# Kernel tuning notes

Measured on AMD Instinct MI355X. Metric: run time of the kernel, lower is better.

Reference implementation:

```python
import jax, jax.numpy as jnp
import numpy as np

N = 10000   # nodes
E = 50000   # edges
C = 64      # in_channels / hidden
OUT = 64    # final out_channels


def _conv(x, src, dst, edge_attr, nn_w, nn_b, lin_w, bias):
    # edge MLP -> per-edge weight matrix [E, C, C]
    W = (edge_attr @ nn_w + nn_b).reshape(-1, C, C)
    x_j = x[src]                                   # gather source features [E, C]
    msg = jnp.einsum('ei,eio->eo', x_j, W)         # batched matvec [E, C]
    out = jax.ops.segment_sum(msg, dst, num_segments=N)  # scatter-add to targets
    out = out + x @ lin_w + bias                   # root weight + bias
    return out


def setup_inputs() -> dict:
    key = jax.random.key(0)
    ks = jax.random.split(key, 13)
    s = 1.0 / np.sqrt(C).astype(np.float32)
    return {
        'feature': jax.random.normal(ks[0], (N, C), dtype=jnp.float32),
        'edge_index': jax.random.randint(ks[1], (2, E), 0, N),
        'edge_attr': jax.random.normal(ks[2], (E, C), dtype=jnp.float32),
        # conv layer 0 (in=64 -> out=64)
        'nn_w0': jax.random.normal(ks[3], (C, C * C), dtype=jnp.float32) * s,
        'nn_b0': jnp.zeros((C * C,), dtype=jnp.float32),
        'lin_w0': jax.random.normal(ks[4], (C, C), dtype=jnp.float32) * s,
        'bias0': jnp.zeros((C,), dtype=jnp.float32),
        # conv layer 1 (64 -> 64)
        'nn_w1': jax.random.normal(ks[5], (C, C * C), dtype=jnp.float32) * s,
        'nn_b1': jnp.zeros((C * C,), dtype=jnp.float32),
        'lin_w1': jax.random.normal(ks[6], (C, C), dtype=jnp.float32) * s,
        'bias1': jnp.zeros((C,), dtype=jnp.float32),
        # final linear 64 -> 64
        'fin_w': jax.random.normal(ks[7], (C, OUT), dtype=jnp.float32) * s,
        'fin_b': jnp.zeros((OUT,), dtype=jnp.float32),
    }


def reference(feature, edge_index, edge_attr,
              nn_w0, nn_b0, lin_w0, bias0,
              nn_w1, nn_b1, lin_w1, bias1,
              fin_w, fin_b):
    src, dst = edge_index[0], edge_index[1]  # PyG flow: source_to_target
    x = jax.nn.relu(_conv(feature, src, dst, edge_attr, nn_w0, nn_b0, lin_w0, bias0))
    x = jax.nn.relu(_conv(x, src, dst, edge_attr, nn_w1, nn_b1, lin_w1, bias1))
    return x @ fin_w + fin_b
```

## Files before the change

kernel.cpp:

```cpp
#include <hip/hip_runtime.h>


#define NNODES 10000
#define NEDGES 50000
#define CH 64
#define NSTAGES 65
#define MW 64

typedef _Float16 f16;
typedef f16 f16x8 __attribute__((ext_vector_type(8)));
typedef float f32x4 __attribute__((ext_vector_type(4)));


__global__ void zero_kernel(int* __restrict__ hist, int* __restrict__ cursor) {
    int idx = blockIdx.x * 256 + threadIdx.x;
    if (idx < NNODES) { hist[idx] = 0; cursor[idx] = 0; }
}

__global__ void hist_kernel(const int* __restrict__ ei, int* __restrict__ hist) {
    int e = blockIdx.x * 256 + threadIdx.x;
    if (e < NEDGES) atomicAdd(&hist[ei[NEDGES + e]], 1);
}

__global__ __launch_bounds__(1024)
void scan_kernel(const int* __restrict__ hist, int* __restrict__ start) {
    __shared__ int buf[1024];
    int t = threadIdx.x;
    int base = t * 10;
    int loc[10];
    int s = 0;
#pragma unroll
    for (int i = 0; i < 10; ++i) {
        int n = base + i;
        int v = (n < NNODES) ? hist[n] : 0;
        loc[i] = s; s += v;
    }
    buf[t] = s;
    __syncthreads();
    for (int off = 1; off < 1024; off <<= 1) {
        int add = (t >= off) ? buf[t - off] : 0;
        __syncthreads();
        buf[t] += add;
        __syncthreads();
    }
    int ebase = buf[t] - s;
#pragma unroll
    for (int i = 0; i < 10; ++i) {
        int n = base + i;
        if (n < NNODES) start[n] = ebase + loc[i];
    }
    if (t == 1023) start[NNODES] = buf[1023];
}

__global__ void perm_kernel(const int* __restrict__ ei,
                            const int* __restrict__ start,
                            int* __restrict__ cursor,
                            int* __restrict__ eperm,
                            int* __restrict__ esrc) {
    int e = blockIdx.x * 256 + threadIdx.x;
    if (e < NEDGES) {
        int d = ei[NEDGES + e];
        int pos = start[d] + atomicAdd(&cursor[d], 1);
        eperm[pos] = e;
        esrc[pos]  = ei[e];
    }
}

__global__ void eagather_kernel(const float* __restrict__ ea,
                                const int* __restrict__ eperm,
                                float* __restrict__ eas) {
    int idx = blockIdx.x * 256 + threadIdx.x;
    if (idx >= NEDGES * 16) return;
    int p = idx >> 4, quad = idx & 15;
    int e = eperm[p];
    *(float4*)(eas + (size_t)p * 64 + quad * 4) =
        *(const float4*)(ea + (size_t)e * 64 + quad * 4);
}

__global__ void pack_b_kernel(const float* __restrict__ nw0, const float* __restrict__ nb0,
                              const float* __restrict__ nw1, const float* __restrict__ nb1,
                              f16* __restrict__ Bp0, f16* __restrict__ Bp1) {
    int idx = blockIdx.x * 256 + threadIdx.x;
    if (idx >= 2 * NSTAGES * 2048) return;
    int layer = (idx >= NSTAGES * 2048) ? 1 : 0;
    int r = idx - layer * NSTAGES * 2048;
    const float* nn_w = layer ? nw1 : nw0;
    const float* nn_b = layer ? nb1 : nb0;
    f16* Bp = layer ? Bp1 : Bp0;
    int p  = r & 3;
    int f  = r >> 2;
    int ln = f & 63;
    int q2 = (f >> 6) & 7;
    int s  = f >> 9;
    int tn = q2 >> 1, h = q2 & 1;
    int col  = tn * 16 + (ln & 15);
    int koff = h * 32 + (ln >> 4) * 8 + p * 2;
    float v0, v1;
    if (s < 64) {
        v0 = nn_w[(size_t)koff * 4096 + s * 64 + col];
        v1 = nn_w[(size_t)(koff + 1) * 4096 + s * 64 + col];
    } else {
        v0 = nn_b[koff * 64 + col];
        v1 = nn_b[(koff + 1) * 64 + col];
    }
    union { f16 h2[2]; unsigned u; } pk;
    pk.h2[0] = (f16)v0; pk.h2[1] = (f16)v1;
    *(unsigned*)((char*)Bp + (size_t)f * 16 + p * 4) = pk.u;
}

template<bool RELU_IN>
__global__ __launch_bounds__(64, 2)
void edge_gemm_kernel(const float* __restrict__ x,
                      const int* __restrict__ esrc,
                      const float* __restrict__ eas,
                      const f16* __restrict__ Bp,
                      float* __restrict__ msg) {
    __shared__ f16 xjS[MW][72];

    int ln  = threadIdx.x;
    int l15 = ln & 15, l4 = ln >> 4;
    int e0  = blockIdx.x * MW;
    int nh  = blockIdx.y;

#pragma unroll
    for (int r = 0; r < 16; ++r) {
        int idx = r * 64 + ln;
        int el = idx >> 4, ip = idx & 15;
        int p  = e0 + el;
        float4 v = {0.f, 0.f, 0.f, 0.f};
        if (p < NEDGES)
            v = *(const float4*)(x + (size_t)esrc[p] * CH + ip * 4);
        if (RELU_IN) {
            v.x = fmaxf(v.x, 0.f); v.y = fmaxf(v.y, 0.f);
            v.z = fmaxf(v.z, 0.f); v.w = fmaxf(v.w, 0.f);
        }
        union { f16 h4[4]; uint2 u; } pk;
        pk.h4[0] = (f16)v.x; pk.h4[1] = (f16)v.y;
        pk.h4[2] = (f16)v.z; pk.h4[3] = (f16)v.w;
        *(uint2*)&xjS[el][ip * 4] = pk.u;
    }

    f16x8 eav[4][2];
#pragma unroll
    for (int ms = 0; ms < 4; ++ms) {
        int p = e0 + ms * 16 + l15;
#pragma unroll
        for (int h = 0; h < 2; ++h) {
            float4 a = {0.f,0.f,0.f,0.f}, b = {0.f,0.f,0.f,0.f};
            if (p < NEDGES) {
                const float4* q = (const float4*)(eas + (size_t)p * CH + h * 32 + l4 * 8);
                a = q[0]; b = q[1];
            }
            f16x8 f;
            f[0]=(f16)a.x; f[1]=(f16)a.y; f[2]=(f16)a.z; f[3]=(f16)a.w;
            f[4]=(f16)b.x; f[5]=(f16)b.y; f[6]=(f16)b.z; f[7]=(f16)b.w;
            eav[ms][h] = f;
        }
    }

    f32x4 acc[4][2];
#pragma unroll
    for (int ms = 0; ms < 4; ++ms)
#pragma unroll
        for (int tl = 0; tl < 2; ++tl)
            acc[ms][tl] = (f32x4){0.f, 0.f, 0.f, 0.f};

    const char* gB = (const char*)Bp + nh * 4096 + ln * 16;

#define LOADB(b, sidx) do {                                                     \
        const char* _p = gB + (size_t)(sidx) * 8192;                            \
        b[0] = *(const f16x8*)(_p);                                             \
        b[1] = *(const f16x8*)(_p + 1024);                                      \
        b[2] = *(const f16x8*)(_p + 2048);                                      \
        b[3] = *(const f16x8*)(_p + 3072);                                      \
    } while (0)

#define COMP(sidx, b) do {                                                      \
        _Pragma("unroll")                                                       \
        for (int ms = 0; ms < 4; ++ms) {                                        \
            f16 xv = xjS[ms * 16 + l15][(sidx)];                                \
            f16x8 xsp = {xv, xv, xv, xv, xv, xv, xv, xv};                       \
            f16x8 a0 = eav[ms][0] * xsp;                                        \
            f16x8 a1 = eav[ms][1] * xsp;                                        \
            _Pragma("unroll")                                                   \
            for (int tl = 0; tl < 2; ++tl) {                                    \
                acc[ms][tl] = __builtin_amdgcn_mfma_f32_16x16x32_f16(a0, b[tl*2+0], acc[ms][tl], 0, 0, 0); \
                acc[ms][tl] = __builtin_amdgcn_mfma_f32_16x16x32_f16(a1, b[tl*2+1], acc[ms][tl], 0, 0, 0); \
            }                                                                   \
        }                                                                       \
    } while (0)

#define WAIT8 do { asm volatile("s_waitcnt vmcnt(8)" ::: "memory");             \
                   __builtin_amdgcn_sched_barrier(0); } while (0)

    f16x8 b0[4], b1[4], b2[4];
    LOADB(b0, 0); LOADB(b1, 1); LOADB(b2, 2);
    asm volatile("s_waitcnt vmcnt(0)" ::: "memory");
    __builtin_amdgcn_sched_barrier(0);

#pragma unroll 1
    for (int s = 0; s < 63; s += 3) {
        WAIT8; COMP(s,     b0); LOADB(b0, s + 3);
        WAIT8; COMP(s + 1, b1); LOADB(b1, s + 4);
        WAIT8; COMP(s + 2, b2); LOADB(b2, min(s + 5, 64));
    }
    WAIT8;
    COMP(63, b0);
    asm volatile("s_waitcnt vmcnt(4)" ::: "memory");
    __builtin_amdgcn_sched_barrier(0);
#pragma unroll
    for (int ms = 0; ms < 4; ++ms)
#pragma unroll
        for (int h = 0; h < 2; ++h) {
            f16x8 af = *(const f16x8*)&xjS[ms * 16 + l15][h * 32 + l4 * 8];
#pragma unroll
            for (int tl = 0; tl < 2; ++tl)
                acc[ms][tl] = __builtin_amdgcn_mfma_f32_16x16x32_f16(af, b1[tl * 2 + h], acc[ms][tl], 0, 0, 0);
        }

#pragma unroll
    for (int ms = 0; ms < 4; ++ms)
#pragma unroll
        for (int q = 0; q < 4; ++q) {
            int p = e0 + ms * 16 + l4 * 4 + q;
            if (p < NEDGES) {
                float* row = msg + (size_t)p * CH + nh * 32;
                row[l15]      = acc[ms][0][q];
                row[16 + l15] = acc[ms][1][q];
            }
        }
#undef LOADB
#undef COMP
#undef WAIT8
}

template<bool RELU_IN>
__global__ __launch_bounds__(256)
void rootreduce_kernel(const float* __restrict__ x,
                       const float* __restrict__ lw,
                       const float* __restrict__ bias,
                       const float* __restrict__ msg,
                       const int* __restrict__ start,
                       float* __restrict__ outb) {
    int o  = threadIdx.x & 63;
    int gw = (blockIdx.x * 256 + threadIdx.x) >> 6;
    float lwc[64];
#pragma unroll
    for (int k = 0; k < 64; ++k) lwc[k] = lw[k * 64 + o];
    float bo = bias[o];
    for (int n = gw; n < NNODES; n += 1024) {
        const float4* xr = (const float4*)(x + (size_t)n * 64);
        float acc = bo;
#pragma unroll
        for (int kq = 0; kq < 16; ++kq) {
            float4 xv = xr[kq];
            float a = xv.x, b = xv.y, c = xv.z, d = xv.w;
            if (RELU_IN) {
                a = fmaxf(a, 0.f); b = fmaxf(b, 0.f);
                c = fmaxf(c, 0.f); d = fmaxf(d, 0.f);
            }
            acc = fmaf(a, lwc[kq * 4 + 0], acc);
            acc = fmaf(b, lwc[kq * 4 + 1], acc);
            acc = fmaf(c, lwc[kq * 4 + 2], acc);
            acc = fmaf(d, lwc[kq * 4 + 3], acc);
        }
        int pb = start[n], pe = start[n + 1];
        int p = pb;
        for (; p + 4 <= pe; p += 4) {
            float v0 = msg[(size_t)(p + 0) * 64 + o];
            float v1 = msg[(size_t)(p + 1) * 64 + o];
            float v2 = msg[(size_t)(p + 2) * 64 + o];
            float v3 = msg[(size_t)(p + 3) * 64 + o];
            acc += (v0 + v1) + (v2 + v3);
        }
        for (; p < pe; ++p)
            acc += msg[(size_t)p * 64 + o];
        outb[(size_t)n * 64 + o] = acc;
    }
}

__global__ __launch_bounds__(256)
void final_kernel(const float* __restrict__ x,
                  const float* __restrict__ fw,
                  const float* __restrict__ fb,
                  float* __restrict__ out) {
    int o  = threadIdx.x & 63;
    int gw = (blockIdx.x * 256 + threadIdx.x) >> 6;
    float fwc[64];
#pragma unroll
    for (int k = 0; k < 64; ++k) fwc[k] = fw[k * 64 + o];
    float bo = fb[o];
    for (int n = gw; n < NNODES; n += 1024) {
        const float4* xr = (const float4*)(x + (size_t)n * 64);
        float acc = bo;
#pragma unroll
        for (int kq = 0; kq < 16; ++kq) {
            float4 xv = xr[kq];
            acc = fmaf(fmaxf(xv.x, 0.f), fwc[kq * 4 + 0], acc);
            acc = fmaf(fmaxf(xv.y, 0.f), fwc[kq * 4 + 1], acc);
            acc = fmaf(fmaxf(xv.z, 0.f), fwc[kq * 4 + 2], acc);
            acc = fmaf(fmaxf(xv.w, 0.f), fwc[kq * 4 + 3], acc);
        }
        out[(size_t)n * 64 + o] = acc;
    }
}

extern "C" void kernel_launch(void* const* d_in, const int* in_sizes, int n_in,
                              void* d_out, int out_size, void* d_ws, size_t ws_size,
                              hipStream_t stream) {
    const float* feature = (const float*)d_in[0];
    const int*   ei      = (const int*)d_in[1];
    const float* ea      = (const float*)d_in[2];
    const float* nn_w0   = (const float*)d_in[3];
    const float* nn_b0   = (const float*)d_in[4];
    const float* lin_w0  = (const float*)d_in[5];
    const float* bias0   = (const float*)d_in[6];
    const float* nn_w1   = (const float*)d_in[7];
    const float* nn_b1   = (const float*)d_in[8];
    const float* lin_w1  = (const float*)d_in[9];
    const float* bias1   = (const float*)d_in[10];
    const float* fin_w   = (const float*)d_in[11];
    const float* fin_b   = (const float*)d_in[12];
    float* out = (float*)d_out;

    char* ws = (char*)d_ws;
    float* buf0   = (float*)(ws + 0);
    float* buf1   = (float*)(ws + 2560000);
    f16*   Bp0    = (f16*)  (ws + 5120000);
    f16*   Bp1    = (f16*)  (ws + 5652480);
    int*   hist   = (int*)  (ws + 6184960);
    int*   cursor = (int*)  (ws + 6224960);
    int*   startp = (int*)  (ws + 6264960);
    int*   eperm  = (int*)  (ws + 6304976);
    int*   esrc   = (int*)  (ws + 6504976);
    float* eas    = (float*)(ws + 6704976);
    float* msg    = (float*)(ws + 19504976);

    zero_kernel<<<(NNODES + 255) / 256, 256, 0, stream>>>(hist, cursor);
    hist_kernel<<<(NEDGES + 255) / 256, 256, 0, stream>>>(ei, hist);
    scan_kernel<<<1, 1024, 0, stream>>>(hist, startp);
    perm_kernel<<<(NEDGES + 255) / 256, 256, 0, stream>>>(ei, startp, cursor, eperm, esrc);
    eagather_kernel<<<(NEDGES * 16 + 255) / 256, 256, 0, stream>>>(ea, eperm, eas);

    pack_b_kernel<<<(2 * NSTAGES * 2048 + 255) / 256, 256, 0, stream>>>(
        nn_w0, nn_b0, nn_w1, nn_b1, Bp0, Bp1);

    dim3 eg((NEDGES + MW - 1) / MW, 2);

    edge_gemm_kernel<false><<<eg, 64, 0, stream>>>(feature, esrc, eas, Bp0, msg);
    rootreduce_kernel<false><<<256, 256, 0, stream>>>(feature, lin_w0, bias0,
                                                      msg, startp, buf0);
    edge_gemm_kernel<true><<<eg, 64, 0, stream>>>(buf0, esrc, eas, Bp1, msg);
    rootreduce_kernel<true><<<256, 256, 0, stream>>>(buf0, lin_w1, bias1,
                                                     msg, startp, buf1);
    final_kernel<<<256, 256, 0, stream>>>(buf1, fin_w, fin_b, out);
}
```

Before: 174.6 us.

## Fuse edge-attr gather into perm, final linear into rootreduce, memset zeroing

The edge-attribute gather now happens inside the permutation kernel, so eperm and the separate gather kernel are gone. The final 64x64 linear is fused into the second root/reduce kernel: each wave stages its relu'd row in shared memory and computes the output directly, removing the buf1 round trip and one launch. Zeroing now uses hipMemsetAsync instead of a custom kernel. The cost is that each perm thread copies 256 bytes serially with less coalescing, and the fused kernel holds more registers (fwc[64]). Wave-local shared-memory use without a barrier relies on lockstep execution within a 64-wide wave.

```diff
diff --git a/kernel.cpp b/kernel.cpp
--- a/kernel.cpp
+++ b/kernel.cpp
@@ -11,11 +11,6 @@
 typedef f16 f16x8 __attribute__((ext_vector_type(8)));
 typedef float f32x4 __attribute__((ext_vector_type(4)));
 
-
-__global__ void zero_kernel(int* __restrict__ hist, int* __restrict__ cursor) {
-    int idx = blockIdx.x * 256 + threadIdx.x;
-    if (idx < NNODES) { hist[idx] = 0; cursor[idx] = 0; }
-}
 
 __global__ void hist_kernel(const int* __restrict__ ei, int* __restrict__ hist) {
     int e = blockIdx.x * 256 + threadIdx.x;
@@ -55,26 +50,19 @@
 __global__ void perm_kernel(const int* __restrict__ ei,
                             const int* __restrict__ start,
                             int* __restrict__ cursor,
-                            int* __restrict__ eperm,
-                            int* __restrict__ esrc) {
+                            int* __restrict__ esrc,
+                            const float* __restrict__ ea,
+                            float* __restrict__ eas) {
     int e = blockIdx.x * 256 + threadIdx.x;
     if (e < NEDGES) {
         int d = ei[NEDGES + e];
         int pos = start[d] + atomicAdd(&cursor[d], 1);
-        eperm[pos] = e;
-        esrc[pos]  = ei[e];
-    }
-}
-
-__global__ void eagather_kernel(const float* __restrict__ ea,
-                                const int* __restrict__ eperm,
-                                float* __restrict__ eas) {
-    int idx = blockIdx.x * 256 + threadIdx.x;
-    if (idx >= NEDGES * 16) return;
-    int p = idx >> 4, quad = idx & 15;
-    int e = eperm[p];
-    *(float4*)(eas + (size_t)p * 64 + quad * 4) =
-        *(const float4*)(ea + (size_t)e * 64 + quad * 4);
+        esrc[pos] = ei[e];
+        const float4* src = (const float4*)(ea + (size_t)e * 64);
+        float4* dst = (float4*)(eas + (size_t)pos * 64);
+#pragma unroll
+        for (int q = 0; q < 16; ++q) dst[q] = src[q];
+    }
 }
 
 __global__ void pack_b_kernel(const float* __restrict__ nw0, const float* __restrict__ nb0,
@@ -234,19 +222,30 @@
 #undef WAIT8
 }
 
-template<bool RELU_IN>
+template<bool RELU_IN, bool FINAL>
 __global__ __launch_bounds__(256)
 void rootreduce_kernel(const float* __restrict__ x,
                        const float* __restrict__ lw,
                        const float* __restrict__ bias,
                        const float* __restrict__ msg,
                        const int* __restrict__ start,
+                       const float* __restrict__ fw,
+                       const float* __restrict__ fb,
                        float* __restrict__ outb) {
+    __shared__ float vrow[4][64];
     int o  = threadIdx.x & 63;
+    int wv = threadIdx.x >> 6;
     int gw = (blockIdx.x * 256 + threadIdx.x) >> 6;
     float lwc[64];
 #pragma unroll
     for (int k = 0; k < 64; ++k) lwc[k] = lw[k * 64 + o];
+    float fwc[64];
+    float fbo = 0.f;
+    if (FINAL) {
+#pragma unroll
+        for (int k = 0; k < 64; ++k) fwc[k] = fw[k * 64 + o];
+        fbo = fb[o];
+    }
     float bo = bias[o];
     for (int n = gw; n < NNODES; n += 1024) {
         const float4* xr = (const float4*)(x + (size_t)n * 64);
@@ -275,33 +274,16 @@
         }
         for (; p < pe; ++p)
             acc += msg[(size_t)p * 64 + o];
-        outb[(size_t)n * 64 + o] = acc;
-    }
-}
-
-__global__ __launch_bounds__(256)
-void final_kernel(const float* __restrict__ x,
-                  const float* __restrict__ fw,
-                  const float* __restrict__ fb,
-                  float* __restrict__ out) {
-    int o  = threadIdx.x & 63;
-    int gw = (blockIdx.x * 256 + threadIdx.x) >> 6;
-    float fwc[64];
-#pragma unroll
-    for (int k = 0; k < 64; ++k) fwc[k] = fw[k * 64 + o];
-    float bo = fb[o];
-    for (int n = gw; n < NNODES; n += 1024) {
-        const float4* xr = (const float4*)(x + (size_t)n * 64);
-        float acc = bo;
-#pragma unroll
-        for (int kq = 0; kq < 16; ++kq) {
-            float4 xv = xr[kq];
-            acc = fmaf(fmaxf(xv.x, 0.f), fwc[kq * 4 + 0], acc);
-            acc = fmaf(fmaxf(xv.y, 0.f), fwc[kq * 4 + 1], acc);
-            acc = fmaf(fmaxf(xv.z, 0.f), fwc[kq * 4 + 2], acc);
-            acc = fmaf(fmaxf(xv.w, 0.f), fwc[kq * 4 + 3], acc);
-        }
-        out[(size_t)n * 64 + o] = acc;
+        if (FINAL) {
+            vrow[wv][o] = fmaxf(acc, 0.f);
+            float a2 = fbo;
+#pragma unroll
+            for (int k = 0; k < 64; ++k)
+                a2 = fmaf(vrow[wv][k], fwc[k], a2);
+            outb[(size_t)n * 64 + o] = a2;
+        } else {
+            outb[(size_t)n * 64 + o] = acc;
+        }
     }
 }
 
@@ -325,22 +307,21 @@
 
     char* ws = (char*)d_ws;
     float* buf0   = (float*)(ws + 0);
-    float* buf1   = (float*)(ws + 2560000);
-    f16*   Bp0    = (f16*)  (ws + 5120000);
-    f16*   Bp1    = (f16*)  (ws + 5652480);
-    int*   hist   = (int*)  (ws + 6184960);
-    int*   cursor = (int*)  (ws + 6224960);
-    int*   startp = (int*)  (ws + 6264960);
-    int*   eperm  = (int*)  (ws + 6304976);
-    int*   esrc   = (int*)  (ws + 6504976);
-    float* eas    = (float*)(ws + 6704976);
-    float* msg    = (float*)(ws + 19504976);
-
-    zero_kernel<<<(NNODES + 255) / 256, 256, 0, stream>>>(hist, cursor);
+    f16*   Bp0    = (f16*)  (ws + 2560000);
+    f16*   Bp1    = (f16*)  (ws + 3092480);
+    int*   hist   = (int*)  (ws + 3624960);
+    int*   cursor = (int*)  (ws + 3664960);
+    int*   startp = (int*)  (ws + 3704960);
+    int*   esrc   = (int*)  (ws + 3744976);
+    float* eas    = (float*)(ws + 3944976);
+    float* msg    = (float*)(ws + 16744976);
+
+    hipMemsetAsync(hist, 0, NNODES * sizeof(int), stream);
+    hipMemsetAsync(cursor, 0, NNODES * sizeof(int), stream);
     hist_kernel<<<(NEDGES + 255) / 256, 256, 0, stream>>>(ei, hist);
     scan_kernel<<<1, 1024, 0, stream>>>(hist, startp);
-    perm_kernel<<<(NEDGES + 255) / 256, 256, 0, stream>>>(ei, startp, cursor, eperm, esrc);
-    eagather_kernel<<<(NEDGES * 16 + 255) / 256, 256, 0, stream>>>(ea, eperm, eas);
+    perm_kernel<<<(NEDGES + 255) / 256, 256, 0, stream>>>(ei, startp, cursor,
+                                                          esrc, ea, eas);
 
     pack_b_kernel<<<(2 * NSTAGES * 2048 + 255) / 256, 256, 0, stream>>>(
         nn_w0, nn_b0, nn_w1, nn_b1, Bp0, Bp1);
@@ -348,10 +329,9 @@
     dim3 eg((NEDGES + MW - 1) / MW, 2);
 
     edge_gemm_kernel<false><<<eg, 64, 0, stream>>>(feature, esrc, eas, Bp0, msg);
-    rootreduce_kernel<false><<<256, 256, 0, stream>>>(feature, lin_w0, bias0,
-                                                      msg, startp, buf0);
+    rootreduce_kernel<false, false><<<256, 256, 0, stream>>>(
+        feature, lin_w0, bias0, msg, startp, fin_w, fin_b, buf0);
     edge_gemm_kernel<true><<<eg, 64, 0, stream>>>(buf0, esrc, eas, Bp1, msg);
-    rootreduce_kernel<true><<<256, 256, 0, stream>>>(buf0, lin_w1, bias1,
-                                                     msg, startp, buf1);
-    final_kernel<<<256, 256, 0, stream>>>(buf1, fin_w, fin_b, out);
-}
+    rootreduce_kernel<true, true><<<256, 256, 0, stream>>>(
+        buf0, lin_w1, bias1, msg, startp, fin_w, fin_b, out);
+}
```

Result: faster. 166.1 us (-4.9%).
